# Optimization experiments

Hardware: AMD Instinct MI355X
Metric: run time of the kernel (lower is better)

Reference implementation:

```python
import jax, jax.numpy as jnp
import numpy as np

N = 8192
F = 128

def setup_inputs() -> dict:
    key = jax.random.key(0)
    k1, k2, k3 = jax.random.split(key, 3)
    x = jax.random.normal(k1, (N, F), dtype=jnp.float32)
    adj = jax.random.uniform(k2, (N, N), dtype=jnp.float32)
    # xavier-uniform style init for weight [F, F]
    limit = float(np.sqrt(6.0 / (F + F)))
    weight = jax.random.uniform(k3, (F, F), dtype=jnp.float32, minval=-limit, maxval=limit)
    return {"x": x, "adj": adj, "weight": weight}

def reference(x, adj, weight):
    # adj_hat = adj + I
    n = adj.shape[0]
    adj_hat = adj + jnp.eye(n, dtype=adj.dtype)
    # degree vector; D^{-1/2} A_hat D^{-1/2} expressed as row/col scaling
    deg = jnp.sum(adj_hat, axis=1)
    d_inv_sqrt = (deg + 1e-8) ** -0.5  # [N]
    support = d_inv_sqrt[:, None] * adj_hat * d_inv_sqrt[None, :]  # [N, N]
    out = jnp.matmul(jnp.matmul(support, x), weight)  # [N, F]
    return jax.nn.relu(out)
```

## Files before the change

### kernel.cpp

```cpp
#include <hip/hip_runtime.h>
#include <hip/hip_bf16.h>

#define NN 8192
#define FF 128
#define BM 64
#define BK 64
#define KS 8
#define KCH (NN / KS)
#define NSTEP (KCH / BK)

typedef __attribute__((ext_vector_type(8))) short bf16x8;
typedef __attribute__((ext_vector_type(4))) float f32x4;

__device__ __forceinline__ short f2bf(float f) {
  unsigned u = __float_as_uint(f);
  u += 0x7FFFu + ((u >> 16) & 1u);
  return (short)(u >> 16);
}
__device__ __forceinline__ float bf2f(short s) {
  return __uint_as_float(((unsigned)(unsigned short)s) << 16);
}

__global__ __launch_bounds__(256) void k_deg_cvt(const float* __restrict__ adj,
                                                 float* __restrict__ dinv,
                                                 short* __restrict__ abf) {
  const int row = blockIdx.x;
  const float4* p = (const float4*)(adj + (size_t)row * NN);
  short4* q = (short4*)(abf + (size_t)row * NN);
  float s = 0.f;
#pragma unroll
  for (int it = 0; it < 8; ++it) {
    float4 v = p[it * 256 + threadIdx.x];
    s += (v.x + v.y) + (v.z + v.w);
    short4 o;
    o.x = f2bf(v.x); o.y = f2bf(v.y); o.z = f2bf(v.z); o.w = f2bf(v.w);
    q[it * 256 + threadIdx.x] = o;
  }
#pragma unroll
  for (int off = 32; off > 0; off >>= 1) s += __shfl_down(s, off, 64);
  __shared__ float partial[4];
  if ((threadIdx.x & 63) == 0) partial[threadIdx.x >> 6] = s;
  __syncthreads();
  if (threadIdx.x == 0) {
    float deg = (partial[0] + partial[1]) + (partial[2] + partial[3]) + 1.0f;
    dinv[row] = 1.0f / sqrtf(deg + 1e-8f);
  }
}

__global__ __launch_bounds__(256) void k_scale_t(const float* __restrict__ x,
                                                 const float* __restrict__ dinv,
                                                 short* __restrict__ yT) {
  __shared__ float tile[64][129];
  const int r0 = blockIdx.x * 64;
  const int tid = threadIdx.x;
#pragma unroll
  for (int it = 0; it < 8; ++it) {
    int q = it * 256 + tid;
    int r = q >> 5;
    int c = q & 31;
    float4 v = ((const float4*)(x + (size_t)(r0 + r) * FF))[c];
    float d = dinv[r0 + r];
    tile[r][c * 4 + 0] = v.x * d;
    tile[r][c * 4 + 1] = v.y * d;
    tile[r][c * 4 + 2] = v.z * d;
    tile[r][c * 4 + 3] = v.w * d;
  }
  __syncthreads();
  const int f = tid >> 1;
  const int i0 = (tid & 1) * 32;
#pragma unroll
  for (int g = 0; g < 4; ++g) {
    bf16x8 o;
#pragma unroll
    for (int j = 0; j < 8; ++j) o[j] = f2bf(tile[i0 + g * 8 + j][f]);
    *(bf16x8*)(yT + (size_t)f * NN + r0 + i0 + g * 8) = o;
  }
}

__global__ __launch_bounds__(512, 4) void k_gemm(const short* __restrict__ abf,
                                                 const short* __restrict__ yT,
                                                 short* __restrict__ zpart) {
  __shared__ short As[BM][72];
  __shared__ short Bs[128][72];
  const int tid = threadIdx.x;
  const int wave = tid >> 6;
  const int lane = tid & 63;
  const int mb = 127 - (int)(blockIdx.x & 127);
  const int ks = blockIdx.x >> 7;
  const int row0 = mb * BM;
  const size_t kbase = (size_t)ks * KCH;

  const int s_ar = tid >> 3;
  const int s_ac = (tid & 7) * 8;
  const short* pa  = abf + (size_t)(row0 + s_ar) * NN + kbase + s_ac;
  const short* pb0 = yT + (size_t)s_ar * NN + kbase + s_ac;
  const short* pb1 = yT + (size_t)(s_ar + 64) * NN + kbase + s_ac;

  const int wm = (wave >> 2) * 32;
  const int wn = (wave & 3) * 32;
  const int fr = lane & 15;
  const int kh = (lane >> 4) * 8;

  f32x4 acc00 = {0.f,0.f,0.f,0.f}, acc01 = acc00, acc10 = acc00, acc11 = acc00;

  bf16x8 aX, aY, bX0, bX1, bY0, bY1;

#define LOADT(av, b0v, b1v, koff) do {                                         \
    av  = *(const bf16x8*)(pa  + (koff));                                      \
    b0v = *(const bf16x8*)(pb0 + (koff));                                      \
    b1v = *(const bf16x8*)(pb1 + (koff));                                      \
  } while (0)

#define STAGE(av, b0v, b1v) do {                                               \
    *(bf16x8*)&As[s_ar][s_ac] = av;                                            \
    *(bf16x8*)&Bs[s_ar][s_ac] = b0v;                                           \
    *(bf16x8*)&Bs[s_ar + 64][s_ac] = b1v;                                      \
  } while (0)

#define COMPUTE() do {                                                         \
    _Pragma("unroll")                                                          \
    for (int kk = 0; kk < 2; ++kk) {                                           \
      bf16x8 a0 = *(const bf16x8*)&As[wm + fr][kk * 32 + kh];                  \
      bf16x8 a1 = *(const bf16x8*)&As[wm + 16 + fr][kk * 32 + kh];             \
      bf16x8 b0 = *(const bf16x8*)&Bs[wn + fr][kk * 32 + kh];                  \
      bf16x8 b1 = *(const bf16x8*)&Bs[wn + 16 + fr][kk * 32 + kh];             \
      acc00 = __builtin_amdgcn_mfma_f32_16x16x32_bf16(a0, b0, acc00, 0, 0, 0); \
      acc01 = __builtin_amdgcn_mfma_f32_16x16x32_bf16(a0, b1, acc01, 0, 0, 0); \
      acc10 = __builtin_amdgcn_mfma_f32_16x16x32_bf16(a1, b0, acc10, 0, 0, 0); \
      acc11 = __builtin_amdgcn_mfma_f32_16x16x32_bf16(a1, b1, acc11, 0, 0, 0); \
    }                                                                          \
  } while (0)

  LOADT(aX, bX0, bX1, 0);
  LOADT(aY, bY0, bY1, BK);

  for (int step = 0; step < NSTEP; step += 2) {
    STAGE(aX, bX0, bX1);
    __syncthreads();
    if (step + 2 < NSTEP) LOADT(aX, bX0, bX1, (step + 2) * BK);
    COMPUTE();
    __syncthreads();

    STAGE(aY, bY0, bY1);
    __syncthreads();
    if (step + 3 < NSTEP) LOADT(aY, bY0, bY1, (step + 3) * BK);
    COMPUTE();
    __syncthreads();
  }

  const int r4 = (lane >> 4) * 4;
  short* zp = zpart + ((size_t)ks << 20);
#pragma unroll
  for (int r = 0; r < 4; ++r) {
    int gi0 = row0 + wm + r4 + r;
    int gi1 = gi0 + 16;
    zp[(size_t)gi0 * FF + wn + fr]      = f2bf(acc00[r]);
    zp[(size_t)gi0 * FF + wn + 16 + fr] = f2bf(acc01[r]);
    zp[(size_t)gi1 * FF + wn + fr]      = f2bf(acc10[r]);
    zp[(size_t)gi1 * FF + wn + 16 + fr] = f2bf(acc11[r]);
  }
#undef LOADT
#undef STAGE
#undef COMPUTE
}

__global__ __launch_bounds__(256) void k_out(const short* __restrict__ zpart,
                                             const float* __restrict__ x,
                                             const float* __restrict__ dinv,
                                             const float* __restrict__ w,
                                             float* __restrict__ out) {
  __shared__ float zs[16][128];
  const int r0 = blockIdx.x * 16;
  const int tid = threadIdx.x;
#pragma unroll
  for (int half = 0; half < 2; ++half) {
    int p = half * 256 + tid;
    int r = p >> 5;
    int c4 = p & 31;
    int gi = r0 + r;
    const short* base = zpart + (size_t)gi * FF + c4 * 4;
    float s0 = 0.f, s1 = 0.f, s2 = 0.f, s3 = 0.f;
#pragma unroll
    for (int sidx = 0; sidx < KS; ++sidx) {
      short4 v = *(const short4*)(base + ((size_t)sidx << 20));
      s0 += bf2f(v.x); s1 += bf2f(v.y); s2 += bf2f(v.z); s3 += bf2f(v.w);
    }
    float4 xv = *(const float4*)(x + (size_t)gi * FF + c4 * 4);
    float di = dinv[gi];
    float di2 = di * di;
    zs[r][c4 * 4 + 0] = di * s0 + di2 * xv.x;
    zs[r][c4 * 4 + 1] = di * s1 + di2 * xv.y;
    zs[r][c4 * 4 + 2] = di * s2 + di2 * xv.z;
    zs[r][c4 * 4 + 3] = di * s3 + di2 * xv.w;
  }
  __syncthreads();
  const int f = tid & 127;
  const int rg = (tid >> 7) * 8;
  float acc[8] = {0.f, 0.f, 0.f, 0.f, 0.f, 0.f, 0.f, 0.f};
#pragma unroll 4
  for (int k = 0; k < 128; ++k) {
    float wv = w[k * FF + f];
#pragma unroll
    for (int r = 0; r < 8; ++r) acc[r] += zs[rg + r][k] * wv;
  }
#pragma unroll
  for (int r = 0; r < 8; ++r) {
    out[(size_t)(r0 + rg + r) * FF + f] = fmaxf(acc[r], 0.0f);
  }
}

extern "C" void kernel_launch(void* const* d_in, const int* in_sizes, int n_in,
                              void* d_out, int out_size, void* d_ws, size_t ws_size,
                              hipStream_t stream) {
  const float* x   = (const float*)d_in[0];
  const float* adj = (const float*)d_in[1];
  const float* w   = (const float*)d_in[2];
  float* out = (float*)d_out;

  float* dinv  = (float*)d_ws;
  short* yT    = (short*)((char*)d_ws + 64 * 1024);
  short* zpart = (short*)((char*)d_ws + 4 * 1024 * 1024);
  short* abf   = (short*)((char*)d_ws + 24 * 1024 * 1024);

  k_deg_cvt<<<NN,      256, 0, stream>>>(adj, dinv, abf);
  k_scale_t<<<NN / 64, 256, 0, stream>>>(x, dinv, yT);
  k_gemm   <<<128 * KS, 512, 0, stream>>>(abf, yT, zpart);
  k_out    <<<NN / 16, 256, 0, stream>>>(zpart, x, dinv, w, out);
}
```

Before: 136.8 us.

## Fuse bf16 conversion of adjacency into GEMM and double-buffer LDS tiles

The degree kernel no longer writes a bf16 copy of the adjacency matrix. The GEMM instead loads fp32 adjacency tiles directly and converts them to bf16 when staging them into shared memory. This removes a large intermediate write plus its later re-read. The GEMM main loop also switches to two LDS buffers, which halves the number of block barriers per pair of k-steps. In exchange, the GEMM reads twice as many bytes for the A operand, the conversion work moves into the inner loop, and the larger LDS footprint may lower occupancy.

```diff
diff --git a/kernel.cpp b/kernel.cpp
--- a/kernel.cpp
+++ b/kernel.cpp
@@ -21,20 +21,15 @@
   return __uint_as_float(((unsigned)(unsigned short)s) << 16);
 }
 
-__global__ __launch_bounds__(256) void k_deg_cvt(const float* __restrict__ adj,
-                                                 float* __restrict__ dinv,
-                                                 short* __restrict__ abf) {
+__global__ __launch_bounds__(256) void k_deg(const float* __restrict__ adj,
+                                             float* __restrict__ dinv) {
   const int row = blockIdx.x;
   const float4* p = (const float4*)(adj + (size_t)row * NN);
-  short4* q = (short4*)(abf + (size_t)row * NN);
   float s = 0.f;
 #pragma unroll
   for (int it = 0; it < 8; ++it) {
     float4 v = p[it * 256 + threadIdx.x];
     s += (v.x + v.y) + (v.z + v.w);
-    short4 o;
-    o.x = f2bf(v.x); o.y = f2bf(v.y); o.z = f2bf(v.z); o.w = f2bf(v.w);
-    q[it * 256 + threadIdx.x] = o;
   }
 #pragma unroll
   for (int off = 32; off > 0; off >>= 1) s += __shfl_down(s, off, 64);
@@ -77,11 +72,11 @@
   }
 }
 
-__global__ __launch_bounds__(512, 4) void k_gemm(const short* __restrict__ abf,
+__global__ __launch_bounds__(512, 4) void k_gemm(const float* __restrict__ adj,
                                                  const short* __restrict__ yT,
                                                  short* __restrict__ zpart) {
-  __shared__ short As[BM][72];
-  __shared__ short Bs[128][72];
+  __shared__ short As[2][BM][72];
+  __shared__ short Bs[2][128][72];
   const int tid = threadIdx.x;
   const int wave = tid >> 6;
   const int lane = tid & 63;
@@ -92,7 +87,7 @@
 
   const int s_ar = tid >> 3;
   const int s_ac = (tid & 7) * 8;
-  const short* pa  = abf + (size_t)(row0 + s_ar) * NN + kbase + s_ac;
+  const float* pa  = adj + (size_t)(row0 + s_ar) * NN + kbase + s_ac;
   const short* pb0 = yT + (size_t)s_ar * NN + kbase + s_ac;
   const short* pb1 = yT + (size_t)(s_ar + 64) * NN + kbase + s_ac;
 
@@ -103,27 +98,34 @@
 
   f32x4 acc00 = {0.f,0.f,0.f,0.f}, acc01 = acc00, acc10 = acc00, acc11 = acc00;
 
-  bf16x8 aX, aY, bX0, bX1, bY0, bY1;
-
-#define LOADT(av, b0v, b1v, koff) do {                                         \
-    av  = *(const bf16x8*)(pa  + (koff));                                      \
+  float4 aXlo, aXhi, aYlo, aYhi;
+  bf16x8 bX0, bX1, bY0, bY1;
+
+#define LOADT(alo, ahi, b0v, b1v, koff) do {                                   \
+    alo = *(const float4*)(pa + (koff));                                       \
+    ahi = *(const float4*)(pa + (koff) + 4);                                   \
     b0v = *(const bf16x8*)(pb0 + (koff));                                      \
     b1v = *(const bf16x8*)(pb1 + (koff));                                      \
   } while (0)
 
-#define STAGE(av, b0v, b1v) do {                                               \
-    *(bf16x8*)&As[s_ar][s_ac] = av;                                            \
-    *(bf16x8*)&Bs[s_ar][s_ac] = b0v;                                           \
-    *(bf16x8*)&Bs[s_ar + 64][s_ac] = b1v;                                      \
+#define STAGE(BUF, alo, ahi, b0v, b1v) do {                                    \
+    bf16x8 ap_;                                                                \
+    ap_[0] = f2bf(alo.x); ap_[1] = f2bf(alo.y);                                \
+    ap_[2] = f2bf(alo.z); ap_[3] = f2bf(alo.w);                                \
+    ap_[4] = f2bf(ahi.x); ap_[5] = f2bf(ahi.y);                                \
+    ap_[6] = f2bf(ahi.z); ap_[7] = f2bf(ahi.w);                                \
+    *(bf16x8*)&As[BUF][s_ar][s_ac] = ap_;                                      \
+    *(bf16x8*)&Bs[BUF][s_ar][s_ac] = b0v;                                      \
+    *(bf16x8*)&Bs[BUF][s_ar + 64][s_ac] = b1v;                                 \
   } while (0)
 
-#define COMPUTE() do {                                                         \
+#define COMPUTE(BUF) do {                                                      \
     _Pragma("unroll")                                                          \
     for (int kk = 0; kk < 2; ++kk) {                                           \
-      bf16x8 a0 = *(const bf16x8*)&As[wm + fr][kk * 32 + kh];                  \
-      bf16x8 a1 = *(const bf16x8*)&As[wm + 16 + fr][kk * 32 + kh];             \
-      bf16x8 b0 = *(const bf16x8*)&Bs[wn + fr][kk * 32 + kh];                  \
-      bf16x8 b1 = *(const bf16x8*)&Bs[wn + 16 + fr][kk * 32 + kh];             \
+      bf16x8 a0 = *(const bf16x8*)&As[BUF][wm + fr][kk * 32 + kh];             \
+      bf16x8 a1 = *(const bf16x8*)&As[BUF][wm + 16 + fr][kk * 32 + kh];        \
+      bf16x8 b0 = *(const bf16x8*)&Bs[BUF][wn + fr][kk * 32 + kh];             \
+      bf16x8 b1 = *(const bf16x8*)&Bs[BUF][wn + 16 + fr][kk * 32 + kh];        \
       acc00 = __builtin_amdgcn_mfma_f32_16x16x32_bf16(a0, b0, acc00, 0, 0, 0); \
       acc01 = __builtin_amdgcn_mfma_f32_16x16x32_bf16(a0, b1, acc01, 0, 0, 0); \
       acc10 = __builtin_amdgcn_mfma_f32_16x16x32_bf16(a1, b0, acc10, 0, 0, 0); \
@@ -131,20 +133,19 @@
     }                                                                          \
   } while (0)
 
-  LOADT(aX, bX0, bX1, 0);
-  LOADT(aY, bY0, bY1, BK);
+  LOADT(aXlo, aXhi, bX0, bX1, 0);
+  LOADT(aYlo, aYhi, bY0, bY1, BK);
+  STAGE(0, aXlo, aXhi, bX0, bX1);
+  __syncthreads();
 
   for (int step = 0; step < NSTEP; step += 2) {
-    STAGE(aX, bX0, bX1);
+    STAGE(1, aYlo, aYhi, bY0, bY1);
+    if (step + 2 < NSTEP) LOADT(aXlo, aXhi, bX0, bX1, (step + 2) * BK);
+    COMPUTE(0);
     __syncthreads();
-    if (step + 2 < NSTEP) LOADT(aX, bX0, bX1, (step + 2) * BK);
-    COMPUTE();
-    __syncthreads();
-
-    STAGE(aY, bY0, bY1);
-    __syncthreads();
-    if (step + 3 < NSTEP) LOADT(aY, bY0, bY1, (step + 3) * BK);
-    COMPUTE();
+    if (step + 2 < NSTEP) STAGE(0, aXlo, aXhi, bX0, bX1);
+    if (step + 3 < NSTEP) LOADT(aYlo, aYhi, bY0, bY1, (step + 3) * BK);
+    COMPUTE(1);
     __syncthreads();
   }
 
@@ -220,10 +221,9 @@
   float* dinv  = (float*)d_ws;
   short* yT    = (short*)((char*)d_ws + 64 * 1024);
   short* zpart = (short*)((char*)d_ws + 4 * 1024 * 1024);
-  short* abf   = (short*)((char*)d_ws + 24 * 1024 * 1024);
-
-  k_deg_cvt<<<NN,      256, 0, stream>>>(adj, dinv, abf);
+
+  k_deg    <<<NN,      256, 0, stream>>>(adj, dinv);
   k_scale_t<<<NN / 64, 256, 0, stream>>>(x, dinv, yT);
-  k_gemm   <<<128 * KS, 512, 0, stream>>>(abf, yT, zpart);
+  k_gemm   <<<128 * KS, 512, 0, stream>>>(adj, yT, zpart);
   k_out    <<<NN / 16, 256, 0, stream>>>(zpart, x, dinv, w, out);
 }
```

New measurement: 114.4 us. -16.4%, faster.
